# Optimization experiments

Measured on AMD Instinct MI355X. Metric: run time of the kernel, lower is better.

## Reference

```python
import jax, jax.numpy as jnp
import numpy as np

B, N, U = 4, 4096, 512


def setup_inputs() -> dict:
    key = jax.random.key(0)
    ks = jax.random.split(key, 5)
    s = 1.0 / np.sqrt(U)
    return {
        "x": jax.random.normal(ks[0], (B, N, U), dtype=jnp.float32),
        "Wq": jax.random.normal(ks[1], (U, U), dtype=jnp.float32) * s,
        "bq": jnp.zeros((U,), dtype=jnp.float32),
        "Wk": jax.random.normal(ks[2], (U, U), dtype=jnp.float32) * s,
        "bk": jnp.zeros((U,), dtype=jnp.float32),
        "Wv": jax.random.normal(ks[3], (U, U), dtype=jnp.float32) * s,
        "bv": jnp.zeros((U,), dtype=jnp.float32),
        "Wp": jax.random.normal(ks[4], (U, U), dtype=jnp.float32) * s,
        "bp": jnp.zeros((U,), dtype=jnp.float32),
    }


def reference(x, Wq, bq, Wk, bk, Wv, bv, Wp, bp):
    # x: [B, N, U] single-head self-attention with residual
    scale = jnp.asarray(x.shape[-1], jnp.float32) ** -0.5
    q = x @ Wq + bq
    k = x @ Wk + bk
    v = x @ Wv + bv
    scores = jnp.einsum("bnd,bmd->bnm", q, k) * scale  # [B, N, N]
    attn = jax.nn.softmax(scores, axis=-1)
    ctx = jnp.einsum("bnm,bmd->bnd", attn, v)
    return x + (ctx @ Wp + bp)
```

## Files before the change

### kernel.cpp

```cpp
#include <hip/hip_runtime.h>
#include <hip/hip_bf16.h>
#include <hip/hip_fp8.h>
#include <math.h>

#define NB 4
#define NN 4096
#define UU 512

using short8   = __attribute__((ext_vector_type(8))) short;
using bf16x8   = __attribute__((ext_vector_type(8))) __bf16;
using floatx4  = __attribute__((ext_vector_type(4))) float;
using floatx16 = __attribute__((ext_vector_type(16))) float;

__device__ __forceinline__ floatx4 mfma16(short8 a, short8 b, floatx4 c) {
    return __builtin_amdgcn_mfma_f32_16x16x32_bf16(
        __builtin_bit_cast(bf16x8, a), __builtin_bit_cast(bf16x8, b), c, 0, 0, 0);
}
__device__ __forceinline__ floatx16 mfma32f8(long a, long b, floatx16 c) {
    return __builtin_amdgcn_mfma_f32_32x32x16_fp8_fp8(a, b, c, 0, 0, 0);
}

__device__ __forceinline__ unsigned short f2bf(float f) {
    union { float f; unsigned u; } v; v.f = f;
    return (unsigned short)((v.u + 0x7fffu + ((v.u >> 16) & 1u)) >> 16);
}
__device__ __forceinline__ float bf2f(unsigned short s) {
    union { unsigned u; float f; } v; v.u = ((unsigned)s) << 16; return v.f;
}
__device__ __forceinline__ unsigned char f2fp8(float f) {
    __hip_fp8_e4m3 v(f);
    return (unsigned char)v.__x;
}
__device__ __forceinline__ float fp82f(unsigned char c) {
    __hip_fp8_e4m3 v;
    v.__x = (__hip_fp8_storage_t)c;
    return (float)v;
}

#define GLL16(gp, lp) __builtin_amdgcn_global_load_lds( \
    (const __attribute__((address_space(1))) void*)(gp), \
    (__attribute__((address_space(3))) void*)(lp), 16, 0, 0)

__global__ void __launch_bounds__(256) k_cvt_x(const float* __restrict__ x,
                                               unsigned short* __restrict__ xb) {
    int i = (blockIdx.x * 256 + threadIdx.x) * 4;
    float4 v = *(const float4*)(x + i);
    ushort4 o;
    o.x = f2bf(v.x); o.y = f2bf(v.y); o.z = f2bf(v.z); o.w = f2bf(v.w);
    *(ushort4*)(xb + i) = o;
}

__global__ void __launch_bounds__(256) k_cvt_w4(
    const float* __restrict__ W0, const float* __restrict__ W1,
    const float* __restrict__ W2, const float* __restrict__ W3,
    unsigned short* __restrict__ T0, unsigned short* __restrict__ T1,
    unsigned short* __restrict__ T2, unsigned short* __restrict__ T3) {
    const int z = blockIdx.z;
    const float* W = (z == 0) ? W0 : (z == 1) ? W1 : (z == 2) ? W2 : W3;
    unsigned short* T = (z == 0) ? T0 : (z == 1) ? T1 : (z == 2) ? T2 : T3;
    int idx = blockIdx.x * 256 + threadIdx.x;
    int n = idx >> 9, k = idx & 511;
    T[idx] = f2bf(W[k * 512 + n]);
}

__global__ void __launch_bounds__(256, 2) k_proj(
    const unsigned short* __restrict__ Xb,
    const unsigned short* __restrict__ WqT, const unsigned short* __restrict__ WkT,
    const unsigned short* __restrict__ WvT,
    const float* __restrict__ bq, const float* __restrict__ bk, const float* __restrict__ bv,
    unsigned short* __restrict__ Q, unsigned short* __restrict__ K8,
    unsigned char* __restrict__ V8)
{
    __shared__ __align__(16) unsigned short As[128 * 32];
    __shared__ __align__(16) unsigned short Bs[128 * 32];
    const int z = blockIdx.z;
    const unsigned short* WT = (z == 0) ? WqT : (z == 1) ? WkT : WvT;
    const float* bias = (z == 0) ? bq : (z == 1) ? bk : bv;
    const int t = threadIdx.x, wave = t >> 6, lane = t & 63;
    const int quad = lane >> 4, l16 = lane & 15;
    const int m0 = blockIdx.x * 128, n0 = blockIdx.y * 128;
    const int wm = wave >> 1, wn = wave & 1;

    const int srow = wave * 32 + (lane >> 2);
    const int scol = (lane & 3) * 8;
    const unsigned short* gA = Xb + (size_t)(m0 + srow) * UU + scol;
    const unsigned short* gB = WT + (size_t)(n0 + srow) * UU + scol;
    unsigned short* lA = As + wave * 1024;
    unsigned short* lB = Bs + wave * 1024;

    floatx4 acc[4][4] = {};

    for (int k0 = 0; k0 < UU; k0 += 32) {
        GLL16(gA + k0, lA);
        GLL16(gA + k0 + 16 * UU, lA + 512);
        GLL16(gB + k0, lB);
        GLL16(gB + k0 + 16 * UU, lB + 512);
        __syncthreads();
        short8 a[4], b[4];
        #pragma unroll
        for (int i = 0; i < 4; i++)
            a[i] = *(const short8*)(As + (wm * 64 + i * 16 + l16) * 32 + quad * 8);
        #pragma unroll
        for (int j = 0; j < 4; j++)
            b[j] = *(const short8*)(Bs + (wn * 64 + j * 16 + l16) * 32 + quad * 8);
        #pragma unroll
        for (int i = 0; i < 4; i++)
            #pragma unroll
            for (int j = 0; j < 4; j++)
                acc[i][j] = mfma16(a[i], b[j], acc[i][j]);
        __syncthreads();
    }

    #pragma unroll
    for (int j = 0; j < 4; j++) {
        const int n = n0 + wn * 64 + j * 16 + l16;
        const float bv_ = bias[n];
        #pragma unroll
        for (int i = 0; i < 4; i++) {
            const int mb = m0 + wm * 64 + i * 16 + quad * 4;
            const int bb = mb >> 12, tok = mb & (NN - 1);
            if (z == 0) {
                #pragma unroll
                for (int r = 0; r < 4; r++)
                    Q[(size_t)(mb + r) * UU + n] = f2bf(acc[i][j][r] + bv_);
            } else if (z == 1) {
                const size_t base = (size_t)bb * NN * UU + (size_t)(n >> 3) * (NN * 8)
                                  + (size_t)tok * 8 + (n & 7);
                #pragma unroll
                for (int r = 0; r < 4; r++)
                    K8[base + (size_t)r * 8] = f2bf(acc[i][j][r] + bv_);
            } else {
                uchar4 o8;
                o8.x = f2fp8(acc[i][j][0] + bv_);
                o8.y = f2fp8(acc[i][j][1] + bv_);
                o8.z = f2fp8(acc[i][j][2] + bv_);
                o8.w = f2fp8(acc[i][j][3] + bv_);
                *(uchar4*)(V8 + (size_t)bb * NN * UU + (size_t)(tok >> 3) * (UU * 8)
                           + (size_t)n * 8 + (tok & 7)) = o8;
            }
        }
    }
}

__global__ void __launch_bounds__(512, 1) k_flash(
    const unsigned short* __restrict__ Q,
    const unsigned short* __restrict__ K8,
    const unsigned char*  __restrict__ V8,
    unsigned short* __restrict__ ctx)
{
    __shared__ __align__(16) unsigned short Ks[64 * 64 * 8];
    __shared__ __align__(16) unsigned char  Vs[8 * 512 * 8];
    __shared__ __align__(16) float S_lds[64 * 68];
    __shared__ __align__(16) unsigned char P_lds8[64 * 72];
    __shared__ float m_lds[64], l_lds[64], a_lds[64];

    const int b = blockIdx.y;
    const int q0 = blockIdx.x * 64;
    const int t = threadIdx.x;
    const int wave = t >> 6, lane = t & 63, quad = lane >> 4, l16 = lane & 15;
    const int qt = wave >> 1;
    const int kh = wave & 1;
    const int qh = wave >> 2;
    const int dg = wave & 3;
    const int l31 = lane & 31, hi = lane >> 5;

    if (t < 64) { m_lds[t] = -INFINITY; l_lds[t] = 0.f; }

    const unsigned short* qp = Q + (size_t)(b * NN + q0 + qt * 16 + l16) * UU + quad * 8;
    short8 qf[16];
    #pragma unroll
    for (int kk = 0; kk < 16; kk++) qf[kk] = *(const short8*)(qp + kk * 32);

    const unsigned short* K8b = K8 + (size_t)b * NN * UU;
    const unsigned char*  V8b = V8 + (size_t)b * NN * UU;

    #pragma unroll
    for (int j = 0; j < 8; j++) {
        const int dc = wave * 8 + j;
        GLL16(K8b + (size_t)dc * (NN * 8) + lane * 8, Ks + dc * 512 + lane * 8);
    }

    floatx16 o[4] = {};
    const float sscale = 0.04419417382415922f * 1.4426950408889634f;

    __syncthreads();

    for (int kt = 0; kt < NN; kt += 64) {
        #pragma unroll
        for (int j = 0; j < 4; j++) {
            const int c = wave * 4 + j;
            GLL16(V8b + (size_t)kt * 512 + (size_t)c * 1024 + lane * 16,
                  Vs + c * 1024 + lane * 16);
        }

        floatx4 s0 = {}, s1 = {};
        #pragma unroll
        for (int kk = 0; kk < 16; kk++) {
            const unsigned short* kb = Ks + (kk * 4 + quad) * 512 + (kh * 32 + l16) * 8;
            short8 b0 = *(const short8*)(kb);
            short8 b1 = *(const short8*)(kb + 128);
            s0 = mfma16(qf[kk], b0, s0);
            s1 = mfma16(qf[kk], b1, s1);
        }
        #pragma unroll
        for (int i = 0; i < 4; i++) {
            S_lds[(qt * 16 + quad * 4 + i) * 68 + kh * 32 + l16]      = s0[i] * sscale;
            S_lds[(qt * 16 + quad * 4 + i) * 68 + kh * 32 + 16 + l16] = s1[i] * sscale;
        }
        __syncthreads();

        {
            const int row = t >> 3, c8 = (t & 7) * 8;
            const float4* sp = (const float4*)(S_lds + row * 68 + c8);
            float4 va = sp[0], vb = sp[1];
            float mx = fmaxf(fmaxf(fmaxf(va.x, va.y), fmaxf(va.z, va.w)),
                             fmaxf(fmaxf(vb.x, vb.y), fmaxf(vb.z, vb.w)));
            mx = fmaxf(mx, __shfl_xor(mx, 1, 8));
            mx = fmaxf(mx, __shfl_xor(mx, 2, 8));
            mx = fmaxf(mx, __shfl_xor(mx, 4, 8));
            const float m_old = m_lds[row];
            const float m_new = fmaxf(m_old, mx);
            float p[8] = { exp2f(va.x - m_new), exp2f(va.y - m_new),
                           exp2f(va.z - m_new), exp2f(va.w - m_new),
                           exp2f(vb.x - m_new), exp2f(vb.y - m_new),
                           exp2f(vb.z - m_new), exp2f(vb.w - m_new) };
            unsigned long long pv8 = 0ull; float sum = 0.f;
            #pragma unroll
            for (int j = 0; j < 8; j++) {
                unsigned char uc = f2fp8(p[j]);
                pv8 |= (unsigned long long)uc << (8 * j);
                sum += fp82f(uc);
            }
            *(unsigned long long*)(P_lds8 + row * 72 + c8) = pv8;
            sum += __shfl_xor(sum, 1, 8);
            sum += __shfl_xor(sum, 2, 8);
            sum += __shfl_xor(sum, 4, 8);
            if ((t & 7) == 0) {
                const float alpha = exp2f(m_old - m_new);
                a_lds[row] = alpha;
                m_lds[row] = m_new;
                l_lds[row] = l_lds[row] * alpha + sum;
            }
        }
        __syncthreads();

        if (kt + 64 < NN) {
            #pragma unroll
            for (int j = 0; j < 8; j++) {
                const int dc = wave * 8 + j;
                GLL16(K8b + (size_t)dc * (NN * 8) + (size_t)(kt + 64 + lane) * 8,
                      Ks + dc * 512 + lane * 8);
            }
        }

        {
            float4 al4[4];
            #pragma unroll
            for (int r1 = 0; r1 < 4; r1++)
                al4[r1] = *(const float4*)(a_lds + qh * 32 + hi * 4 + r1 * 8);
            #pragma unroll
            for (int tt = 0; tt < 4; tt++)
                #pragma unroll
                for (int r = 0; r < 16; r++)
                    o[tt][r] *= al4[r >> 2][r & 3];

            long aP[4];
            #pragma unroll
            for (int ks = 0; ks < 4; ks++)
                aP[ks] = *(const long*)(P_lds8 + (qh * 32 + l31) * 72 + ks * 16 + hi * 8);
            #pragma unroll
            for (int ks = 0; ks < 4; ks++) {
                #pragma unroll
                for (int tt = 0; tt < 4; tt++) {
                    const int d0 = dg * 128 + tt * 32;
                    long bV = *(const long*)(Vs + (ks * 2 + hi) * 4096
                                             + (size_t)(d0 + l31) * 8);
                    o[tt] = mfma32f8(aP[ks], bV, o[tt]);
                }
            }
        }
        __syncthreads();
    }

    float4 li4[4];
    #pragma unroll
    for (int r1 = 0; r1 < 4; r1++) {
        float4 lv = *(const float4*)(l_lds + qh * 32 + hi * 4 + r1 * 8);
        li4[r1] = make_float4(1.f / lv.x, 1.f / lv.y, 1.f / lv.z, 1.f / lv.w);
    }
    #pragma unroll
    for (int tt = 0; tt < 4; tt++) {
        const int d0 = dg * 128 + tt * 32;
        #pragma unroll
        for (int r = 0; r < 16; r++) {
            const int row = q0 + qh * 32 + (r & 3) + 8 * (r >> 2) + 4 * hi;
            ctx[(size_t)(b * NN + row) * UU + d0 + l31]
                = f2bf(o[tt][r] * ((const float*)&li4[r >> 2])[r & 3]);
        }
    }
}

__global__ void __launch_bounds__(256, 2) k_out(
    const unsigned short* __restrict__ Cx,
    const unsigned short* __restrict__ WpT,
    const float* __restrict__ bp,
    const float* __restrict__ x,
    float* __restrict__ out)
{
    __shared__ __align__(16) unsigned short As[128 * 32];
    __shared__ __align__(16) unsigned short Bs[128 * 32];
    const int t = threadIdx.x, wave = t >> 6, lane = t & 63;
    const int quad = lane >> 4, l16 = lane & 15;
    const int m0 = blockIdx.x * 128, n0 = blockIdx.y * 128;
    const int wm = wave >> 1, wn = wave & 1;
    const int srow = wave * 32 + (lane >> 2);
    const int scol = (lane & 3) * 8;
    const unsigned short* gA = Cx + (size_t)(m0 + srow) * UU + scol;
    const unsigned short* gB = WpT + (size_t)(n0 + srow) * UU + scol;
    unsigned short* lA = As + wave * 1024;
    unsigned short* lB = Bs + wave * 1024;

    floatx4 acc[4][4] = {};

    for (int k0 = 0; k0 < UU; k0 += 32) {
        GLL16(gA + k0, lA);
        GLL16(gA + k0 + 16 * UU, lA + 512);
        GLL16(gB + k0, lB);
        GLL16(gB + k0 + 16 * UU, lB + 512);
        __syncthreads();
        short8 a[4], b[4];
        #pragma unroll
        for (int i = 0; i < 4; i++)
            a[i] = *(const short8*)(As + (wm * 64 + i * 16 + l16) * 32 + quad * 8);
        #pragma unroll
        for (int j = 0; j < 4; j++)
            b[j] = *(const short8*)(Bs + (wn * 64 + j * 16 + l16) * 32 + quad * 8);
        #pragma unroll
        for (int i = 0; i < 4; i++)
            #pragma unroll
            for (int j = 0; j < 4; j++)
                acc[i][j] = mfma16(a[i], b[j], acc[i][j]);
        __syncthreads();
    }

    #pragma unroll
    for (int j = 0; j < 4; j++) {
        const int n = n0 + wn * 64 + j * 16 + l16;
        const float bv_ = bp[n];
        #pragma unroll
        for (int i = 0; i < 4; i++) {
            const int mb = m0 + wm * 64 + i * 16 + quad * 4;
            #pragma unroll
            for (int r = 0; r < 4; r++) {
                const size_t idx = (size_t)(mb + r) * UU + n;
                out[idx] = acc[i][j][r] + bv_ + x[idx];
            }
        }
    }
}

extern "C" void kernel_launch(void* const* d_in, const int* in_sizes, int n_in,
                              void* d_out, int out_size, void* d_ws, size_t ws_size,
                              hipStream_t stream)
{
    const float* x  = (const float*)d_in[0];
    const float* Wq = (const float*)d_in[1];
    const float* bq = (const float*)d_in[2];
    const float* Wk = (const float*)d_in[3];
    const float* bk = (const float*)d_in[4];
    const float* Wv = (const float*)d_in[5];
    const float* bv = (const float*)d_in[6];
    const float* Wp = (const float*)d_in[7];
    const float* bp = (const float*)d_in[8];
    float* out = (float*)d_out;

    char* ws = (char*)d_ws;
    unsigned short* Xb  = (unsigned short*)(ws);
    unsigned short* WqT = (unsigned short*)(ws + 16777216);
    unsigned short* WkT = (unsigned short*)(ws + 17301504);
    unsigned short* WvT = (unsigned short*)(ws + 17825792);
    unsigned short* WpT = (unsigned short*)(ws + 18350080);
    unsigned short* Qm  = (unsigned short*)(ws + 18874368);
    unsigned short* K8m = (unsigned short*)(ws + 35651584);
    unsigned char*  V8m = (unsigned char*)(ws + 52428800);
    unsigned short* Cx  = (unsigned short*)(ws + 69206016);

    hipLaunchKernelGGL(k_cvt_x, dim3(8192), dim3(256), 0, stream, x, Xb);
    hipLaunchKernelGGL(k_cvt_w4, dim3(1024, 1, 4), dim3(256), 0, stream,
                       Wq, Wk, Wv, Wp, WqT, WkT, WvT, WpT);
    hipLaunchKernelGGL(k_proj, dim3(128, 4, 3), dim3(256), 0, stream,
                       Xb, WqT, WkT, WvT, bq, bk, bv, Qm, K8m, V8m);
    hipLaunchKernelGGL(k_flash, dim3(64, 4), dim3(512), 0, stream, Qm, K8m, V8m, Cx);
    hipLaunchKernelGGL(k_out, dim3(128, 4), dim3(256), 0, stream, Cx, WpT, bp, x, out);
}
```

Before: 354.0 us.

## Store Q and K in FP8 and compute QK^T with FP8 MFMA

Q and K are now emitted as FP8 e4m3 by the projection kernel instead of bf16. The attention kernel computes scores with 16x16x32 FP8 MFMA, which halves K tile traffic and the register footprint of the Q fragments. The K prefetch for the next tile also moves earlier, right after the scores are written, so the load overlaps the softmax. This gives up score accuracy because QK^T is now done in FP8, and the earlier prefetch overwrites the K tile right after a barrier, which relies on every wave having finished reading it.

```diff
diff --git a/kernel.cpp b/kernel.cpp
--- a/kernel.cpp
+++ b/kernel.cpp
@@ -15,6 +15,9 @@
 __device__ __forceinline__ floatx4 mfma16(short8 a, short8 b, floatx4 c) {
     return __builtin_amdgcn_mfma_f32_16x16x32_bf16(
         __builtin_bit_cast(bf16x8, a), __builtin_bit_cast(bf16x8, b), c, 0, 0, 0);
+}
+__device__ __forceinline__ floatx4 mfma16f8(long a, long b, floatx4 c) {
+    return __builtin_amdgcn_mfma_f32_16x16x32_fp8_fp8(a, b, c, 0, 0, 0);
 }
 __device__ __forceinline__ floatx16 mfma32f8(long a, long b, floatx16 c) {
     return __builtin_amdgcn_mfma_f32_32x32x16_fp8_fp8(a, b, c, 0, 0, 0);
@@ -68,7 +71,7 @@
     const unsigned short* __restrict__ WqT, const unsigned short* __restrict__ WkT,
     const unsigned short* __restrict__ WvT,
     const float* __restrict__ bq, const float* __restrict__ bk, const float* __restrict__ bv,
-    unsigned short* __restrict__ Q, unsigned short* __restrict__ K8,
+    unsigned char* __restrict__ Q, unsigned char* __restrict__ K8,
     unsigned char* __restrict__ V8)
 {
     __shared__ __align__(16) unsigned short As[128 * 32];
@@ -122,13 +125,13 @@
             if (z == 0) {
                 #pragma unroll
                 for (int r = 0; r < 4; r++)
-                    Q[(size_t)(mb + r) * UU + n] = f2bf(acc[i][j][r] + bv_);
+                    Q[(size_t)(mb + r) * UU + n] = f2fp8(acc[i][j][r] + bv_);
             } else if (z == 1) {
                 const size_t base = (size_t)bb * NN * UU + (size_t)(n >> 3) * (NN * 8)
                                   + (size_t)tok * 8 + (n & 7);
                 #pragma unroll
                 for (int r = 0; r < 4; r++)
-                    K8[base + (size_t)r * 8] = f2bf(acc[i][j][r] + bv_);
+                    K8[base + (size_t)r * 8] = f2fp8(acc[i][j][r] + bv_);
             } else {
                 uchar4 o8;
                 o8.x = f2fp8(acc[i][j][0] + bv_);
@@ -143,13 +146,13 @@
 }
 
 __global__ void __launch_bounds__(512, 1) k_flash(
-    const unsigned short* __restrict__ Q,
-    const unsigned short* __restrict__ K8,
-    const unsigned char*  __restrict__ V8,
+    const unsigned char* __restrict__ Q,
+    const unsigned char* __restrict__ K8,
+    const unsigned char* __restrict__ V8,
     unsigned short* __restrict__ ctx)
 {
-    __shared__ __align__(16) unsigned short Ks[64 * 64 * 8];
-    __shared__ __align__(16) unsigned char  Vs[8 * 512 * 8];
+    __shared__ __align__(16) unsigned char Ks[64 * 64 * 8];
+    __shared__ __align__(16) unsigned char Vs[8 * 512 * 8];
     __shared__ __align__(16) float S_lds[64 * 68];
     __shared__ __align__(16) unsigned char P_lds8[64 * 72];
     __shared__ float m_lds[64], l_lds[64], a_lds[64];
@@ -166,18 +169,19 @@
 
     if (t < 64) { m_lds[t] = -INFINITY; l_lds[t] = 0.f; }
 
-    const unsigned short* qp = Q + (size_t)(b * NN + q0 + qt * 16 + l16) * UU + quad * 8;
-    short8 qf[16];
-    #pragma unroll
-    for (int kk = 0; kk < 16; kk++) qf[kk] = *(const short8*)(qp + kk * 32);
-
-    const unsigned short* K8b = K8 + (size_t)b * NN * UU;
-    const unsigned char*  V8b = V8 + (size_t)b * NN * UU;
-
-    #pragma unroll
-    for (int j = 0; j < 8; j++) {
-        const int dc = wave * 8 + j;
-        GLL16(K8b + (size_t)dc * (NN * 8) + lane * 8, Ks + dc * 512 + lane * 8);
+    const unsigned char* qp = Q + (size_t)(b * NN + q0 + qt * 16 + l16) * UU + quad * 8;
+    long qf[16];
+    #pragma unroll
+    for (int kk = 0; kk < 16; kk++) qf[kk] = *(const long*)(qp + kk * 32);
+
+    const unsigned char* K8b = K8 + (size_t)b * NN * UU;
+    const unsigned char* V8b = V8 + (size_t)b * NN * UU;
+
+    #pragma unroll
+    for (int j = 0; j < 4; j++) {
+        const int dc = wave * 8 + j * 2;
+        GLL16(K8b + (size_t)(dc + (lane >> 5)) * (NN * 8) + (size_t)((lane & 31) * 2) * 8,
+              Ks + dc * 512 + lane * 16);
     }
 
     floatx16 o[4] = {};
@@ -196,11 +200,11 @@
         floatx4 s0 = {}, s1 = {};
         #pragma unroll
         for (int kk = 0; kk < 16; kk++) {
-            const unsigned short* kb = Ks + (kk * 4 + quad) * 512 + (kh * 32 + l16) * 8;
-            short8 b0 = *(const short8*)(kb);
-            short8 b1 = *(const short8*)(kb + 128);
-            s0 = mfma16(qf[kk], b0, s0);
-            s1 = mfma16(qf[kk], b1, s1);
+            const unsigned char* kb = Ks + ((kk * 4 + quad) * 64 + kh * 32 + l16) * 8;
+            long b0 = *(const long*)(kb);
+            long b1 = *(const long*)(kb + 128);
+            s0 = mfma16f8(qf[kk], b0, s0);
+            s1 = mfma16f8(qf[kk], b1, s1);
         }
         #pragma unroll
         for (int i = 0; i < 4; i++) {
@@ -208,6 +212,16 @@
             S_lds[(qt * 16 + quad * 4 + i) * 68 + kh * 32 + 16 + l16] = s1[i] * sscale;
         }
         __syncthreads();
+
+        if (kt + 64 < NN) {
+            #pragma unroll
+            for (int j = 0; j < 4; j++) {
+                const int dc = wave * 8 + j * 2;
+                GLL16(K8b + (size_t)(dc + (lane >> 5)) * (NN * 8)
+                          + (size_t)(kt + 64 + (lane & 31) * 2) * 8,
+                      Ks + dc * 512 + lane * 16);
+            }
+        }
 
         {
             const int row = t >> 3, c8 = (t & 7) * 8;
@@ -243,15 +257,6 @@
             }
         }
         __syncthreads();
-
-        if (kt + 64 < NN) {
-            #pragma unroll
-            for (int j = 0; j < 8; j++) {
-                const int dc = wave * 8 + j;
-                GLL16(K8b + (size_t)dc * (NN * 8) + (size_t)(kt + 64 + lane) * 8,
-                      Ks + dc * 512 + lane * 8);
-            }
-        }
 
         {
             float4 al4[4];
@@ -380,8 +385,8 @@
     unsigned short* WkT = (unsigned short*)(ws + 17301504);
     unsigned short* WvT = (unsigned short*)(ws + 17825792);
     unsigned short* WpT = (unsigned short*)(ws + 18350080);
-    unsigned short* Qm  = (unsigned short*)(ws + 18874368);
-    unsigned short* K8m = (unsigned short*)(ws + 35651584);
+    unsigned char*  Qm  = (unsigned char*)(ws + 18874368);
+    unsigned char*  K8m = (unsigned char*)(ws + 35651584);
     unsigned char*  V8m = (unsigned char*)(ws + 52428800);
     unsigned short* Cx  = (unsigned short*)(ws + 69206016);
 
```

Result: faster. 344.0 us (-2.8%).
